# Optimization experiments

Hardware: AMD Instinct MI355X
Metric: run time of the kernel (lower is better)

The kernel has to match this reference:

```python
import jax, jax.numpy as jnp
import numpy as np

SEQ_LEN = 16384
D = 2048
K = 50          # tagset size
START = 48
STOP = 49
NEG = -10000.0


def setup_inputs() -> dict:
    key = jax.random.key(0)
    k1, k2, k3, k4 = jax.random.split(key, 4)
    input_var = jax.random.normal(k1, (SEQ_LEN, D), jnp.float32)
    tags = jax.random.randint(k2, (SEQ_LEN,), 0, 48, dtype=jnp.int32)  # real tags only
    W = jax.random.normal(k3, (K, D), jnp.float32) * 0.02              # hidden2tag weight
    b = jnp.zeros((K,), jnp.float32)                                   # hidden2tag bias
    transitions = jax.random.normal(k4, (K, K), jnp.float32) * 0.1
    # match the torch init: no transition into START, none out of STOP
    transitions = transitions.at[START, :].set(NEG).at[:, STOP].set(NEG)
    return {"input_var": input_var, "tags": tags, "W": W, "b": b, "transitions": transitions}


def reference(input_var, tags, W, b, transitions):
    # dropout in eval mode == identity (faithful deterministic forward)
    feats = input_var @ W.T + b  # [T, K] emission scores

    # --- CRF forward algorithm (log partition) ---
    alpha0 = jnp.full((K,), NEG, jnp.float32).at[START].set(0.0)

    def step(alpha, feat):
        # tag_var[i, j] = alpha[j] + transitions[i, j] + feat[i]
        s = alpha[None, :] + transitions           # [K, K]
        m = jnp.max(s, axis=1)                     # stable log-sum-exp
        alpha_new = feat + m + jnp.log(jnp.sum(jnp.exp(s - m[:, None]), axis=1))
        return alpha_new, None

    alpha, _ = jax.lax.scan(step, alpha0, feats)
    term = alpha + transitions[STOP]
    mt = jnp.max(term)
    forward_score = mt + jnp.log(jnp.sum(jnp.exp(term - mt)))

    # --- gold path score ---
    pad_start = jnp.concatenate([jnp.array([START], dtype=tags.dtype), tags])
    pad_stop = jnp.concatenate([tags, jnp.array([STOP], dtype=tags.dtype)])
    gold = (jnp.sum(transitions[pad_stop, pad_start])
            + jnp.sum(feats[jnp.arange(SEQ_LEN), tags]))

    return forward_score - gold
```

## Files before the change

### kernel.cpp

```cpp
#include <hip/hip_runtime.h>

typedef unsigned short u16;
typedef unsigned int u32;
typedef __bf16 b16x8 __attribute__((ext_vector_type(8)));
typedef float f32x16 __attribute__((ext_vector_type(16)));

#define SEQ   16384
#define DM    2048
#define KT    50
#define NST   48
#define NSP   49

__device__ __forceinline__ int perm64(int g){
  int q = (g>>2)&3;
  return (q==1 || q==2) ? (g^12) : g;
}
__device__ __forceinline__ u16 bfb(float f){
  __bf16 b = (__bf16)f;
  return __builtin_bit_cast(u16, b);
}
__device__ __forceinline__ int pk2(float a, float b){
  return (int)((u32)bfb(a) | ((u32)bfb(b) << 16));
}
__device__ __forceinline__ b16x8 cast8(int4 v){ return __builtin_bit_cast(b16x8, v); }

__device__ __forceinline__ f32x16 mfma_(b16x8 a, b16x8 b, f32x16 c){
  return __builtin_amdgcn_mfma_f32_32x32x16_bf16(a, b, c, 0, 0, 0);
}

__device__ __forceinline__ void mm64(const b16x8 A[2][4], const b16x8 B[4][2], f32x16 acc[2][2]){
#pragma unroll
  for (int mi=0; mi<2; ++mi)
#pragma unroll
    for (int ni=0; ni<2; ++ni){
      f32x16 a;
#pragma unroll
      for (int q=0;q<16;q++) a[q] = 0.0f;
#pragma unroll
      for (int kt=0; kt<4; ++kt) a = mfma_(A[mi][kt], B[kt][ni], a);
      acc[mi][ni] = a;
    }
}

__device__ __forceinline__ void repack(const f32x16 acc[2][2], b16x8 B[4][2]){
#pragma unroll
  for (int kb=0; kb<4; ++kb){
    const int mi = kb>>1, t = kb&1;
#pragma unroll
    for (int ni=0; ni<2; ++ni){
      int4 dw;
      dw.x = pk2(acc[mi][ni][8*t+0], acc[mi][ni][8*t+1]);
      dw.y = pk2(acc[mi][ni][8*t+2], acc[mi][ni][8*t+3]);
      dw.z = pk2(acc[mi][ni][8*t+4], acc[mi][ni][8*t+5]);
      dw.w = pk2(acc[mi][ni][8*t+6], acc[mi][ni][8*t+7]);
      B[kb][ni] = cast8(dw);
    }
  }
}

template<int PERM>
__device__ __forceinline__ void ident_frags(b16x8 B[4][2], int lane){
  const int h = lane>>5, j0 = lane&31;
#pragma unroll
  for (int kt=0; kt<4; ++kt)
#pragma unroll
    for (int ni=0; ni<2; ++ni){
      const int col = j0 + 32*ni;
      int d[4];
#pragma unroll
      for (int dd=0; dd<4; ++dd){
        int r0 = 16*kt + 8*h + 2*dd, r1 = r0 + 1;
        int p0 = PERM ? perm64(r0) : r0;
        int p1 = PERM ? perm64(r1) : r1;
        d[dd] = (int)((p0==col ? 0x3F80u : 0u) | ((p1==col ? 0x3F80u : 0u) << 16));
      }
      int4 v; v.x=d[0]; v.y=d[1]; v.z=d[2]; v.w=d[3];
      B[kt][ni] = cast8(v);
    }
}

__device__ __forceinline__ float acc_wave_max(const f32x16 acc[2][2]){
  float m = 0.0f;
#pragma unroll
  for (int mi=0;mi<2;mi++)
#pragma unroll
    for (int ni=0;ni<2;ni++)
#pragma unroll
      for (int q=0;q<16;q++) m = fmaxf(m, acc[mi][ni][q]);
#pragma unroll
  for (int o=32;o>=1;o>>=1) m = fmaxf(m, __shfl_xor(m, o, 64));
  return m;
}

template<int PROW>
__device__ __forceinline__ void store_mat_lds(u16* mat, const f32x16 acc[2][2], float inv, int lane){
  const int h = lane>>5, j0 = lane&31;
#pragma unroll
  for (int mi=0;mi<2;mi++)
#pragma unroll
    for (int ni=0;ni<2;ni++)
#pragma unroll
      for (int r=0;r<16;r++){
        int gp = 32*mi + (r&3) + 8*(r>>2) + 4*h;
        int a = PROW ? perm64(gp) : gp;
        int b = perm64(32*ni + j0);
        mat[a*64 + (b ^ ((a&7)<<3))] = bfb(acc[mi][ni][r]*inv);
      }
}
template<int PROW>
__device__ __forceinline__ void store_mat_glob(u16* mat, const f32x16 acc[2][2], float inv, int lane){
  const int h = lane>>5, j0 = lane&31;
#pragma unroll
  for (int mi=0;mi<2;mi++)
#pragma unroll
    for (int ni=0;ni<2;ni++)
#pragma unroll
      for (int r=0;r<16;r++){
        int gp = 32*mi + (r&3) + 8*(r>>2) + 4*h;
        int a = PROW ? perm64(gp) : gp;
        int b = perm64(32*ni + j0);
        mat[a*64 + b] = bfb(acc[mi][ni][r]*inv);
      }
}
__device__ __forceinline__ void load_afrag_lds(const u16* mat, b16x8 A[2][4], int lane){
  const int h = lane>>5, i0 = lane&31;
#pragma unroll
  for (int mi=0;mi<2;mi++)
#pragma unroll
    for (int kt=0;kt<4;kt++){
      int i = 32*mi + i0;
      int cb = (16*kt + 8*h) ^ ((i&7)<<3);
      A[mi][kt] = cast8(*(const int4*)(mat + i*64 + cb));
    }
}
__device__ __forceinline__ void load_afrag_glob(const u16* mat, b16x8 A[2][4], int lane){
  const int h = lane>>5, i0 = lane&31;
#pragma unroll
  for (int mi=0;mi<2;mi++)
#pragma unroll
    for (int kt=0;kt<4;kt++){
      int i = 32*mi + i0;
      A[mi][kt] = cast8(*(const int4*)(mat + i*64 + 16*kt + 8*h));
    }
}

__global__ void k_prep(const float* __restrict__ W, const float* __restrict__ T,
                       u16* __restrict__ Wp, u16* __restrict__ E){
  int tid = blockIdx.x*256 + threadIdx.x;
  int n = gridDim.x*256;
  for (int idx = tid; idx < 64*DM; idx += n){
    int r = idx >> 11, d = idx & 2047;
    Wp[idx] = (r < KT) ? bfb(W[r*DM + d]) : (u16)0;
  }
  for (int idx = tid; idx < 64*64; idx += n){
    int a = idx >> 6, b = idx & 63;
    int pa = perm64(a);
    E[idx] = (pa < KT && b < KT) ? bfb(__expf(T[pa*50 + b])) : (u16)0;
  }
}

__global__ __launch_bounds__(256, 2) void k_gemm(const float* __restrict__ in,
      const u16* __restrict__ Wp, const float* __restrict__ bias,
      const int* __restrict__ tags, float* __restrict__ feats, float* __restrict__ gout){
  const int w = threadIdx.x>>6, lane = threadIdx.x&63;
  const int h = lane>>5, i0 = lane&31;
  const int blk = blockIdx.x;
  const int row = blk*32 + i0;
  f32x16 acc0, acc1;
#pragma unroll
  for (int q=0;q<16;q++){ acc0[q]=0.f; acc1[q]=0.f; }
  const float* pa  = in + (size_t)row*DM + w*512 + 8*h;
  const u16*   pb0 = Wp + (size_t)i0*DM + w*512 + 8*h;
  const u16*   pb1 = Wp + (size_t)(i0+32)*DM + w*512 + 8*h;
#pragma unroll 4
  for (int s=0;s<32;s++){
    float4 fa = *(const float4*)(pa + s*16);
    float4 fb = *(const float4*)(pa + s*16 + 4);
    b16x8 av;
    av[0]=(__bf16)fa.x; av[1]=(__bf16)fa.y; av[2]=(__bf16)fa.z; av[3]=(__bf16)fa.w;
    av[4]=(__bf16)fb.x; av[5]=(__bf16)fb.y; av[6]=(__bf16)fb.z; av[7]=(__bf16)fb.w;
    b16x8 b0 = cast8(*(const int4*)(pb0 + s*16));
    b16x8 b1 = cast8(*(const int4*)(pb1 + s*16));
    acc0 = mfma_(av, b0, acc0);
    acc1 = mfma_(av, b1, acc1);
  }
  __shared__ float planes[4][32][64];
#pragma unroll
  for (int r=0;r<16;r++){
    int g = (r&3) + 8*(r>>2) + 4*h;
    planes[w][g][i0]    = acc0[r];
    planes[w][g][i0+32] = acc1[r];
  }
  __syncthreads();
  __shared__ float tile[32][66];
  for (int cidx = threadIdx.x; cidx < 2048; cidx += 256){
    int g = cidx>>6, c = cidx&63;
    float v = planes[0][g][c]+planes[1][g][c]+planes[2][g][c]+planes[3][g][c];
    tile[g][c] = (c<KT) ? (v + bias[c]) : -1e4f;
  }
  __syncthreads();
  __shared__ float mrow[32];
  if (threadIdx.x < 32){
    int g = threadIdx.x;
    float mx = -1e30f;
    for (int c=0;c<KT;c++) mx = fmaxf(mx, tile[g][c]);
    mrow[g] = mx;
    int t = blk*32 + g;
    gout[t] = tile[g][tags[t]] - mx;
  }
  __syncthreads();
  for (int cidx = threadIdx.x; cidx < 2048; cidx += 256){
    int g = cidx>>6, c = cidx&63;
    feats[(size_t)(blk*32+g)*64 + c] = (c<KT) ? (tile[g][c] - mrow[g]) : -1e4f;
  }
}

__global__ __launch_bounds__(512, 2) void k_scan(const float* __restrict__ feats,
        const u16* __restrict__ Emat, u16* __restrict__ M1, float* __restrict__ S1){
  const int w = threadIdx.x >> 6, lane = threadIdx.x & 63;
  const int h = lane>>5;
  const int blk = blockIdx.x;
  const int t0 = (blk*8 + w)*8;
  __shared__ __align__(16) float u_lds[8][64];
  __shared__ __align__(16) u16 mats[8][4096];
  __shared__ float logs[8];

  b16x8 Af[2][4];
  load_afrag_glob(Emat, Af, lane);
  b16x8 Bf[4][2];
  ident_frags<0>(Bf, lane);
  const int pl = perm64(lane);
  float x = feats[(size_t)t0*64 + pl];
  f32x16 acc[2][2];
#pragma unroll
  for (int s=0;s<8;s++){
    u_lds[w][lane] = __expf(x);
    if (s<7) x = feats[(size_t)(t0+s+1)*64 + pl];
    mm64(Af, Bf, acc);
    float uu0[16], uu1[16];
#pragma unroll
    for (int k2=0;k2<4;k2++){
      float4 v0 = *(const float4*)&u_lds[w][      8*k2 + 4*h];
      float4 v1 = *(const float4*)&u_lds[w][32 +  8*k2 + 4*h];
      uu0[4*k2+0]=v0.x; uu0[4*k2+1]=v0.y; uu0[4*k2+2]=v0.z; uu0[4*k2+3]=v0.w;
      uu1[4*k2+0]=v1.x; uu1[4*k2+1]=v1.y; uu1[4*k2+2]=v1.z; uu1[4*k2+3]=v1.w;
    }
#pragma unroll
    for (int ni=0;ni<2;ni++)
#pragma unroll
      for (int r=0;r<16;r++){
        acc[0][ni][r] *= uu0[r];
        acc[1][ni][r] *= uu1[r];
      }
    repack(acc, Bf);
  }
  float m = acc_wave_max(acc);
  float inv = 1.0f/m;
  store_mat_lds<1>(mats[w], acc, inv, lane);
  if (lane==0) logs[w] = __logf(m);
  __syncthreads();
  if (w==0){
    float slog = logs[0]+logs[1]+logs[2]+logs[3]+logs[4]+logs[5]+logs[6]+logs[7];
    b16x8 Bc[4][2]; ident_frags<1>(Bc, lane);
    f32x16 a2[2][2];
#pragma unroll 1
    for (int m8=0;m8<8;m8++){
      b16x8 Am[2][4];
      load_afrag_lds(mats[m8], Am, lane);
      mm64(Am, Bc, a2);
      repack(a2, Bc);
    }
    float m2 = acc_wave_max(a2);
    slog += __logf(m2);
    store_mat_glob<0>(M1 + (size_t)blk*4096, a2, 1.0f/m2, lane);
    if (lane==0) S1[blk] = slog;
  }
}

__global__ __launch_bounds__(64) void k_comb8(const u16* __restrict__ Min, const float* __restrict__ Sin,
      u16* __restrict__ Mout, float* __restrict__ Sout){
  const int lane = threadIdx.x & 63;
  const int blk = blockIdx.x;
  b16x8 Bc[4][2]; ident_frags<1>(Bc, lane);
  f32x16 a2[2][2];
  float slog = 0.f;
#pragma unroll 1
  for (int m=0;m<8;m++){
    b16x8 Am[2][4];
    load_afrag_glob(Min + (size_t)(blk*8+m)*4096, Am, lane);
    slog += Sin[blk*8+m];
    mm64(Am, Bc, a2);
    repack(a2, Bc);
  }
  float mx = acc_wave_max(a2);
  slog += __logf(mx);
  store_mat_glob<0>(Mout + (size_t)blk*4096, a2, 1.0f/mx, lane);
  if (lane==0) Sout[blk] = slog;
}

__global__ __launch_bounds__(512, 2) void k_final(const u16* __restrict__ M2, const float* __restrict__ S2,
      const float* __restrict__ T, const int* __restrict__ tags,
      const float* __restrict__ gvec, float* __restrict__ out){
  const int w = threadIdx.x>>6, lane = threadIdx.x&63;
  __shared__ __align__(16) u16 mats[8][4096];
  __shared__ float logs[8];
  __shared__ float alpha[64];
  __shared__ float red[512];
  __shared__ float slog_sh;
  {
    b16x8 Bc[4][2]; ident_frags<1>(Bc, lane);
    f32x16 a2[2][2];
    float sl = 0.f;
#pragma unroll 1
    for (int m=0;m<4;m++){
      b16x8 Am[2][4];
      load_afrag_glob(M2 + (size_t)(w*4+m)*4096, Am, lane);
      sl += S2[w*4+m];
      mm64(Am, Bc, a2);
      repack(a2, Bc);
    }
    float mx = acc_wave_max(a2);
    sl += __logf(mx);
    store_mat_lds<0>(mats[w], a2, 1.0f/mx, lane);
    if (lane==0) logs[w] = sl;
  }
  __syncthreads();
  if (w==0){
    b16x8 Bc[4][2]; ident_frags<1>(Bc, lane);
    f32x16 a2[2][2];
#pragma unroll 1
    for (int m=0;m<8;m++){
      b16x8 Am[2][4];
      load_afrag_lds(mats[m], Am, lane);
      mm64(Am, Bc, a2);
      repack(a2, Bc);
    }
    float sl = logs[0]+logs[1]+logs[2]+logs[3]+logs[4]+logs[5]+logs[6]+logs[7];
    if ((lane&31)==16){
      const int h = lane>>5;
#pragma unroll
      for (int mi=0;mi<2;mi++)
#pragma unroll
        for (int r=0;r<16;r++){
          int gp = 32*mi + (r&3) + 8*(r>>2) + 4*h;
          alpha[gp] = a2[mi][1][r];
        }
    }
    if (lane==0) slog_sh = sl;
  }
  float part = 0.f;
  for (int t = threadIdx.x; t < SEQ; t += 512) part += gvec[t];
  for (int idx = threadIdx.x; idx < SEQ+1; idx += 512){
    int s0 = (idx==0) ? NST : tags[idx-1];
    int s1 = (idx<SEQ) ? tags[idx] : NSP;
    part += T[s1*50 + s0];
  }
  red[threadIdx.x] = part;
  for (int st=256; st>0; st>>=1){
    __syncthreads();
    if (threadIdx.x < st) red[threadIdx.x] += red[threadIdx.x + st];
  }
  __syncthreads();
  if (threadIdx.x < 64){
    float a = alpha[lane];
    float term = (lane < KT && a > 0.f) ? (__logf(a) + slog_sh + T[NSP*50 + lane]) : -1e30f;
    float tm = term;
#pragma unroll
    for (int o=32;o>=1;o>>=1) tm = fmaxf(tm, __shfl_xor(tm, o, 64));
    float e = __expf(term - tm);
#pragma unroll
    for (int o=32;o>=1;o>>=1) e += __shfl_xor(e, o, 64);
    if (threadIdx.x == 0) out[0] = (tm + __logf(e)) - red[0];
  }
}

extern "C" void kernel_launch(void* const* d_in, const int* in_sizes, int n_in,
                              void* d_out, int out_size, void* d_ws, size_t ws_size,
                              hipStream_t stream) {
  (void)in_sizes; (void)n_in; (void)out_size; (void)ws_size;
  const float* input = (const float*)d_in[0];
  const int*   tags  = (const int*)  d_in[1];
  const float* W     = (const float*)d_in[2];
  const float* bias  = (const float*)d_in[3];
  const float* T     = (const float*)d_in[4];

  char* ws = (char*)d_ws;
  float* feats = (float*)(ws + 0);
  float* gvec  = (float*)(ws + 4194304);
  u16*   Wp    = (u16*)  (ws + 4259840);
  u16*   Emat  = (u16*)  (ws + 4521984);
  u16*   M1    = (u16*)  (ws + 4530176);
  float* S1    = (float*)(ws + 6627328);
  u16*   M2    = (u16*)  (ws + 6628352);
  float* S2    = (float*)(ws + 6890496);

  k_prep <<<256, 256, 0, stream>>>(W, T, Wp, Emat);
  k_gemm <<<512, 256, 0, stream>>>(input, Wp, bias, tags, feats, gvec);
  k_scan <<<256, 512, 0, stream>>>(feats, Emat, M1, S1);
  k_comb8<<<32,  64,  0, stream>>>(M1, S1, M2, S2);
  k_final<<<1,   512, 0, stream>>>(M2, S2, T, tags, gvec, (float*)d_out);
}
```

Measured before the change: 111.0 us.

## Stage GEMM operands through double-buffered swizzled LDS with async weight loads

The emission GEMM now stages K-chunks of 128 through shared memory. The next chunk's weights are copied with global_load_lds while the input rows are prefetched into registers, converted to bf16 and written to a swizzled buffer. Each wave covers a 32-column half and half of each chunk's K range, and the two partial sums are reduced in LDS at the end. The weight prep kernel pre-swizzles the bf16 weights into a chunked layout to match. This is meant to hide global-load latency and stop each wave re-reading the weights from global memory, at the cost of 48KB LDS per block (which may limit occupancy) and a barrier per chunk.

```diff
diff --git a/kernel.cpp b/kernel.cpp
--- a/kernel.cpp
+++ b/kernel.cpp
@@ -145,12 +145,14 @@
 }
 
 __global__ void k_prep(const float* __restrict__ W, const float* __restrict__ T,
-                       u16* __restrict__ Wp, u16* __restrict__ E){
+                       u16* __restrict__ WpS, u16* __restrict__ E){
   int tid = blockIdx.x*256 + threadIdx.x;
   int n = gridDim.x*256;
-  for (int idx = tid; idx < 64*DM; idx += n){
-    int r = idx >> 11, d = idx & 2047;
-    Wp[idx] = (r < KT) ? bfb(W[r*DM + d]) : (u16)0;
+  for (int idx = tid; idx < 16*8192; idx += n){
+    int kc = idx >> 13, e = idx & 8191;
+    int r = e >> 7, m = e & 127;
+    int kin = m ^ ((r&7)<<3);
+    WpS[idx] = (r < KT) ? bfb(W[r*DM + kc*128 + kin]) : (u16)0;
   }
   for (int idx = tid; idx < 64*64; idx += n){
     int a = idx >> 6, b = idx & 63;
@@ -159,60 +161,119 @@
   }
 }
 
+__device__ __forceinline__ void gll16(const void* g, void* l){
+  __builtin_amdgcn_global_load_lds((const __attribute__((address_space(1))) u32*)g,
+                                   (__attribute__((address_space(3))) u32*)l, 16, 0, 0);
+}
+
 __global__ __launch_bounds__(256, 2) void k_gemm(const float* __restrict__ in,
-      const u16* __restrict__ Wp, const float* __restrict__ bias,
+      const u16* __restrict__ WpS, const float* __restrict__ bias,
       const int* __restrict__ tags, float* __restrict__ feats, float* __restrict__ gout){
-  const int w = threadIdx.x>>6, lane = threadIdx.x&63;
-  const int h = lane>>5, i0 = lane&31;
-  const int blk = blockIdx.x;
-  const int row = blk*32 + i0;
-  f32x16 acc0, acc1;
-#pragma unroll
-  for (int q=0;q<16;q++){ acc0[q]=0.f; acc1[q]=0.f; }
-  const float* pa  = in + (size_t)row*DM + w*512 + 8*h;
-  const u16*   pb0 = Wp + (size_t)i0*DM + w*512 + 8*h;
-  const u16*   pb1 = Wp + (size_t)(i0+32)*DM + w*512 + 8*h;
-#pragma unroll 4
-  for (int s=0;s<32;s++){
-    float4 fa = *(const float4*)(pa + s*16);
-    float4 fb = *(const float4*)(pa + s*16 + 4);
-    b16x8 av;
-    av[0]=(__bf16)fa.x; av[1]=(__bf16)fa.y; av[2]=(__bf16)fa.z; av[3]=(__bf16)fa.w;
-    av[4]=(__bf16)fb.x; av[5]=(__bf16)fb.y; av[6]=(__bf16)fb.z; av[7]=(__bf16)fb.w;
-    b16x8 b0 = cast8(*(const int4*)(pb0 + s*16));
-    b16x8 b1 = cast8(*(const int4*)(pb1 + s*16));
-    acc0 = mfma_(av, b0, acc0);
-    acc1 = mfma_(av, b1, acc1);
-  }
-  __shared__ float planes[4][32][64];
+  __shared__ __align__(16) char smem[49152];
+  u16* const bA = (u16*)smem;
+  u16* const bB = (u16*)(smem + 16384);
+  const int t = threadIdx.x;
+  const int w = t>>6, lane = t&63;
+  const int j0 = lane&31, h = lane>>5;
+  const int wc = w&1, kh = w>>1;
+  const int row0 = blockIdx.x*32;
+
+  const int aswz = (j0&7)<<3;
+  float regA[2][8];
+  f32x16 accE, accO;
+#pragma unroll
+  for (int q=0;q<16;q++){ accE[q]=0.f; accO[q]=0.f; }
+
+#define ISSUE_A(kc)                                                        \
+  {                                                                        \
+    _Pragma("unroll")                                                      \
+    for (int i=0;i<2;i++){                                                 \
+      int g = (i<<8) + t;                                                  \
+      int r = g>>4, c8 = g&15;                                             \
+      const float* p = in + (size_t)(row0 + r)*DM + (kc)*128 + c8*8;       \
+      float4 f0 = *(const float4*)p;                                       \
+      float4 f1 = *(const float4*)(p+4);                                   \
+      regA[i][0]=f0.x; regA[i][1]=f0.y; regA[i][2]=f0.z; regA[i][3]=f0.w;  \
+      regA[i][4]=f1.x; regA[i][5]=f1.y; regA[i][6]=f1.z; regA[i][7]=f1.w;  \
+    }                                                                      \
+  }
+#define WRITE_A(d)                                                         \
+  {                                                                        \
+    _Pragma("unroll")                                                      \
+    for (int i=0;i<2;i++){                                                 \
+      int g = (i<<8) + t;                                                  \
+      int r = g>>4, c8 = g&15;                                             \
+      int4 dw; dw.x = pk2(regA[i][0],regA[i][1]); dw.y = pk2(regA[i][2],regA[i][3]); \
+      dw.z = pk2(regA[i][4],regA[i][5]); dw.w = pk2(regA[i][6],regA[i][7]);\
+      *(int4*)(bA + (d)*4096 + r*128 + ((c8*8) ^ ((r&7)<<3))) = dw;        \
+    }                                                                      \
+  }
+#define ISSUE_B(kc, d)                                                     \
+  {                                                                        \
+    const u16* src = WpS + (kc)*8192 + w*2048 + lane*8;                    \
+    u16* dst = bB + (d)*8192 + w*2048;                                     \
+    _Pragma("unroll")                                                      \
+    for (int i=0;i<4;i++) gll16(src + i*512, dst + i*512);                 \
+  }
+
+  ISSUE_B(0, 0);
+  ISSUE_A(0);
+  WRITE_A(0);
+  __syncthreads();
+
+  for (int kc=0; kc<16; ++kc){
+    const int d = kc & 1;
+    if (kc < 15){ ISSUE_B(kc+1, d^1); ISSUE_A(kc+1); }
+    const u16* Arow  = bA + d*4096 + j0*128;
+    const u16* Brow  = bB + d*8192 + (32*wc + j0)*128;
+#pragma unroll
+    for (int kk=0; kk<2; ++kk){
+      const int ktE = kh*4 + 2*kk, ktO = ktE + 1;
+      b16x8 aE = cast8(*(const int4*)(Arow + ((ktE*16 + h*8) ^ aswz)));
+      b16x8 bE = cast8(*(const int4*)(Brow + ((ktE*16 + h*8) ^ aswz)));
+      accE = mfma_(aE, bE, accE);
+      b16x8 aO = cast8(*(const int4*)(Arow + ((ktO*16 + h*8) ^ aswz)));
+      b16x8 bO = cast8(*(const int4*)(Brow + ((ktO*16 + h*8) ^ aswz)));
+      accO = mfma_(aO, bO, accO);
+    }
+    if (kc < 15) WRITE_A(d^1);
+    __syncthreads();
+  }
+
+  f32x16 accS;
+#pragma unroll
+  for (int q=0;q<16;q++) accS[q] = accE[q] + accO[q];
+  float* planes = (float*)smem;
+  float* tile   = (float*)(smem + 16384);
+  float* mrow   = (float*)(smem + 24832);
 #pragma unroll
   for (int r=0;r<16;r++){
-    int g = (r&3) + 8*(r>>2) + 4*h;
-    planes[w][g][i0]    = acc0[r];
-    planes[w][g][i0+32] = acc1[r];
-  }
-  __syncthreads();
-  __shared__ float tile[32][66];
-  for (int cidx = threadIdx.x; cidx < 2048; cidx += 256){
+    int gp = (r&3) + 8*(r>>2) + 4*h;
+    planes[(kh*32 + gp)*64 + 32*wc + j0] = accS[r];
+  }
+  __syncthreads();
+  for (int cidx = t; cidx < 2048; cidx += 256){
     int g = cidx>>6, c = cidx&63;
-    float v = planes[0][g][c]+planes[1][g][c]+planes[2][g][c]+planes[3][g][c];
-    tile[g][c] = (c<KT) ? (v + bias[c]) : -1e4f;
-  }
-  __syncthreads();
-  __shared__ float mrow[32];
-  if (threadIdx.x < 32){
-    int g = threadIdx.x;
+    float v = planes[g*64+c] + planes[(32+g)*64+c];
+    tile[g*66+c] = (c<KT) ? (v + bias[c]) : -1e4f;
+  }
+  __syncthreads();
+  if (t < 32){
+    int g = t;
     float mx = -1e30f;
-    for (int c=0;c<KT;c++) mx = fmaxf(mx, tile[g][c]);
+    for (int c=0;c<KT;c++) mx = fmaxf(mx, tile[g*66+c]);
     mrow[g] = mx;
-    int t = blk*32 + g;
-    gout[t] = tile[g][tags[t]] - mx;
-  }
-  __syncthreads();
-  for (int cidx = threadIdx.x; cidx < 2048; cidx += 256){
+    int tt = row0 + g;
+    gout[tt] = tile[g*66 + tags[tt]] - mx;
+  }
+  __syncthreads();
+  for (int cidx = t; cidx < 2048; cidx += 256){
     int g = cidx>>6, c = cidx&63;
-    feats[(size_t)(blk*32+g)*64 + c] = (c<KT) ? (tile[g][c] - mrow[g]) : -1e4f;
-  }
+    feats[(size_t)(row0+g)*64 + c] = (c<KT) ? (tile[g*66+c] - mrow[g]) : -1e4f;
+  }
+#undef ISSUE_A
+#undef WRITE_A
+#undef ISSUE_B
 }
 
 __global__ __launch_bounds__(512, 2) void k_scan(const float* __restrict__ feats,
@@ -387,15 +448,15 @@
   char* ws = (char*)d_ws;
   float* feats = (float*)(ws + 0);
   float* gvec  = (float*)(ws + 4194304);
-  u16*   Wp    = (u16*)  (ws + 4259840);
+  u16*   WpS   = (u16*)  (ws + 4259840);
   u16*   Emat  = (u16*)  (ws + 4521984);
   u16*   M1    = (u16*)  (ws + 4530176);
   float* S1    = (float*)(ws + 6627328);
   u16*   M2    = (u16*)  (ws + 6628352);
   float* S2    = (float*)(ws + 6890496);
 
-  k_prep <<<256, 256, 0, stream>>>(W, T, Wp, Emat);
-  k_gemm <<<512, 256, 0, stream>>>(input, Wp, bias, tags, feats, gvec);
+  k_prep <<<256, 256, 0, stream>>>(W, T, WpS, Emat);
+  k_gemm <<<512, 256, 0, stream>>>(input, WpS, bias, tags, feats, gvec);
   k_scan <<<256, 512, 0, stream>>>(feats, Emat, M1, S1);
   k_comb8<<<32,  64,  0, stream>>>(M1, S1, M2, S2);
   k_final<<<1,   512, 0, stream>>>(M2, S2, T, tags, gvec, (float*)d_out);
```

Measured after the change: 115.4 us. 1.04x slower.
